# Performance work log

Measured on AMD Instinct MI355X. Metric: run time of the kernel, lower is better.

## Reference

```python
import jax, jax.numpy as jnp
import numpy as np

# (C,H,W) of x0..x11; flattened size +1 homogeneous coordinate per key
SHAPES = [(3,32,32),(96,32,32),(96,32,32),(96,16,16),(192,16,16),(192,16,16),(192,8,8),(192,8,8),(192,8,8),(640,1,1),(100,1,1),(10,1,1)]
# (Cin,Cout,k,stride,pad) for conv1..conv9
CONV = [(3,96,3,1,1),(96,96,3,1,1),(96,96,3,2,1),(96,192,3,1,1),(192,192,3,1,1),(192,192,3,2,1),(192,192,3,1,1),(192,192,1,1,0),(192,10,1,1,0)]
B = 128


def setup_inputs():
    key = jax.random.key(0)
    inp = {}
    k, key = jax.random.split(key)
    inp['x0'] = jax.random.normal(k, (int(np.prod(SHAPES[0])) + 1, B), jnp.float32)
    for i, s in enumerate(SHAPES):
        n = int(np.prod(s)) + 1
        k1, k2, key = jax.random.split(key, 3)
        inp['perm%d' % i] = jax.random.permutation(k1, n)
        inp['diag%d' % i] = jax.random.uniform(k2, (n,), jnp.float32, 0.5, 1.5)
    for j, (ci, co, ks, st, pd) in enumerate(CONV):
        k1, k2, key = jax.random.split(key, 3)
        inp['w%d' % (j + 1)] = jax.random.normal(k1, (co, ci, ks, ks), jnp.float32) / np.float32(np.sqrt(ci * ks * ks))
        inp['b%d' % (j + 1)] = jax.random.normal(k2, (co,), jnp.float32) * 0.01
    k1, k2, k3, k4 = jax.random.split(key, 4)
    inp['fw1'] = jax.random.normal(k1, (100, 640), jnp.float32) / np.float32(np.sqrt(640))
    inp['fb1'] = jax.random.normal(k2, (100,), jnp.float32) * 0.01
    inp['fw2'] = jax.random.normal(k3, (10, 100), jnp.float32) / np.float32(np.sqrt(100))
    inp['fb2'] = jax.random.normal(k4, (10,), jnp.float32) * 0.01
    return inp


def _decode(x, perm, diag):
    # A_inv @ x with A_inv = P^T D^{-1}; P^T gather index is argsort(perm)
    return (x / diag[:, None])[jnp.argsort(perm)]


def _encode(y, perm, diag):
    # A @ y with A = D P; (P y)[i] = y[perm[i]]
    return diag[:, None] * y[perm]


def _conv_aug(v, w, b, shape_in, stride, pad):
    # affine-augmented conv: [W b; 0 1] applied to [feat; t]
    C, H, Wd = shape_in
    feat, t = v[:-1], v[-1]                      # (C*H*W, B), (B,)
    x = feat.T.reshape(-1, C, H, Wd)
    y = jax.lax.conv_general_dilated(x, w, (stride, stride), [(pad, pad), (pad, pad)],
                                     dimension_numbers=('NCHW', 'OIHW', 'NCHW'))
    y = y + b[None, :, None, None] * t[:, None, None, None]
    yf = y.reshape(y.shape[0], -1).T             # (N_out, B)
    return jnp.concatenate([yf, t[None, :]], axis=0)


def _fc_aug(v, w, b):
    feat, t = v[:-1], v[-1]
    return jnp.concatenate([w @ feat + b[:, None] * t[None, :], t[None, :]], axis=0)


def _forward(x0, perms, diags, ws, bs, fw1, fb1, fw2, fb2):
    x = x0
    for i in range(9):
        v = _decode(x, perms[i], diags[i])
        y = _conv_aug(v, ws[i], bs[i], SHAPES[i], CONV[i][3], CONV[i][4])
        x = jax.nn.relu(_encode(y, perms[i + 1], diags[i + 1]))
    v = _decode(x, perms[9], diags[9])
    x = jax.nn.relu(_encode(_fc_aug(v, fw1, fb1), perms[10], diags[10]))
    v = _decode(x, perms[10], diags[10])
    return _encode(_fc_aug(v, fw2, fb2), perms[11], diags[11])


def reference(x0, perm0, perm1, perm2, perm3, perm4, perm5, perm6, perm7, perm8, perm9, perm10, perm11,
              diag0, diag1, diag2, diag3, diag4, diag5, diag6, diag7, diag8, diag9, diag10, diag11,
              w1, b1, w2, b2, w3, b3, w4, b4, w5, b5, w6, b6, w7, b7, w8, b8, w9, b9,
              fw1, fb1, fw2, fb2):
    perms = [perm0, perm1, perm2, perm3, perm4, perm5, perm6, perm7, perm8, perm9, perm10, perm11]
    diags = [diag0, diag1, diag2, diag3, diag4, diag5, diag6, diag7, diag8, diag9, diag10, diag11]
    ws = [w1, w2, w3, w4, w5, w6, w7, w8, w9]
    bs = [b1, b2, b3, b4, b5, b6, b7, b8, b9]
    return _forward(x0, perms, diags, ws, bs, fw1, fb1, fw2, fb2)
```

## Files before the change

### kernel.cpp

```cpp
#include <hip/hip_runtime.h>
#include <stdint.h>


#define B 128
#define ZPAD 2048
#define NBLK 1024
#define NTHR 256
#define JSTRIDE ((NBLK >> 3) * 4)
#define AGT __HIP_MEMORY_SCOPE_AGENT

typedef _Float16 f16_t;
typedef __attribute__((ext_vector_type(8))) _Float16 f16x8;
typedef __attribute__((ext_vector_type(4))) _Float16 f16x4;
typedef __attribute__((ext_vector_type(4))) float f32x4;

struct WArgs {
    const float* w[9]; const float* b[9];
    int Ci[9], Co[9], KS[9], Cp[9], NCG[9];
    int woff[10]; int boff[10];
};

__device__ __forceinline__ int xcc_id() {
    int x;
    asm("s_getreg_b32 %0, hwreg(20, 0, 32)" : "=s"(x));
    return x & 7;
}

__device__ __forceinline__ void gbar(int* bar, int ph) {
    __syncthreads();
    if (threadIdx.x == 0) {
        const int x = xcc_id();
        int* leaf  = bar + x * 32;
        int* ldone = bar + 256 + x * 32;
        int* root  = bar + 512;
        int* cnt   = bar + 544;
        if (ph == 0) {
            for (;;) {
                int s = 0;
#pragma unroll
                for (int k = 0; k < 8; ++k)
                    s += __hip_atomic_load(cnt + k, __ATOMIC_RELAXED, AGT);
                if (s == NBLK) break;
                __builtin_amdgcn_s_sleep(2);
            }
        }
        const int myc = __hip_atomic_load(cnt + x, __ATOMIC_RELAXED, AGT);
        int nact = 0;
#pragma unroll
        for (int k = 0; k < 8; ++k)
            nact += (__hip_atomic_load(cnt + k, __ATOMIC_RELAXED, AGT) != 0) ? 1 : 0;
        int old = __hip_atomic_fetch_add(leaf, 1, __ATOMIC_RELAXED, AGT);
        if (old == (ph + 1) * myc - 1) {
            __builtin_amdgcn_fence(__ATOMIC_RELEASE, "agent");
            __hip_atomic_fetch_add(root, 1, __ATOMIC_RELAXED, AGT);
            while (__hip_atomic_load(root, __ATOMIC_RELAXED, AGT) < (ph + 1) * nact)
                __builtin_amdgcn_s_sleep(8);
            __builtin_amdgcn_fence(__ATOMIC_ACQUIRE, "agent");
            __hip_atomic_store(ldone, ph + 1, __ATOMIC_RELAXED, AGT);
        } else {
            while (__hip_atomic_load(ldone, __ATOMIC_RELAXED, AGT) < ph + 1)
                __builtin_amdgcn_s_sleep(8);
            asm volatile("buffer_inv sc0\n\ts_waitcnt vmcnt(0)" ::: "memory");
        }
    }
    __syncthreads();
}

__device__ void prep_phase(const WArgs& A,
                           const float* __restrict__ x0, const int* __restrict__ perm0,
                           const float* __restrict__ diag0,
                           f16_t* __restrict__ wp, float* __restrict__ bp,
                           f16_t* __restrict__ x8a, f16_t* __restrict__ x8b,
                           float* __restrict__ t0) {
    const int NT = NBLK * NTHR;
    const int gtid = blockIdx.x * NTHR + threadIdx.x;
    for (int idx = gtid; idx < ZPAD; idx += NT) {
        x8a[idx] = (f16_t)0.f; x8b[idx] = (f16_t)0.f;
    }
    for (int idx = gtid; idx < 1024 * 128; idx += NT) {
        int p = idx >> 7, n = idx & 127;
        f16_t* base = x8a + ZPAD + p * 1024 + n * 8;
        base[3] = (f16_t)0.f;
        *(uint64_t*)(base + 4) = 0ull;
    }
    for (int idx = gtid; idx < A.boff[9]; idx += NT) {
        int l = 0;
        while (idx >= A.boff[l + 1]) ++l;
        int co = idx - A.boff[l];
        bp[idx] = (co < A.Co[l]) ? A.b[l][co] : 0.f;
    }
    for (int idx = gtid; idx < A.woff[9]; idx += NT) {
        int l = 0;
        while (idx >= A.woff[l + 1]) ++l;
        int e = idx - A.woff[l];
        int j = e & 7;
        int t1_ = e >> 3;
        int Cp = A.Cp[l];
        int co = t1_ % Cp;
        int gg = t1_ / Cp;
        int ncg = A.NCG[l];
        int tap = gg / ncg, cg = gg - tap * ncg;
        int ks = A.KS[l];
        int kh = tap / ks, kw = tap - kh * ks;
        int ci = cg * 8 + j;
        float val = 0.f;
        if (co < A.Co[l] && tap < ks * ks && ci < A.Ci[l])
            val = A.w[l][(((size_t)co * A.Ci[l] + ci) * ks + kh) * ks + kw];
        wp[idx] = (f16_t)val;
    }
    for (int idx = gtid; idx < 3073 * B; idx += NT) {
        int row = idx >> 7, n = idx & 127;
        int i = perm0[row];
        float val = x0[(size_t)row * B + n] / diag0[row];
        if (i < 3072) {
            int c = i >> 10, pp = i & 1023;
            x8a[ZPAD + pp * 1024 + n * 8 + c] = (f16_t)val;
        } else {
            t0[n] = val;
        }
    }
}

template <int KS, int NS, int NSPLIT, int CB, bool F32OUT,
          int Hi, int Wo_log2, int HWo, int STRD, int PAD,
          int NCG, int NCHUNK, int KGR, int Co, int Cp>
__device__ __forceinline__ void conv_layer(
    const f16_t* __restrict__ xin, const float* __restrict__ t_in,
    const f16_t* __restrict__ wp, const float* __restrict__ bp,
    f16_t* __restrict__ xout, float* __restrict__ t_out, float* __restrict__ f32out)
{
    constexpr int PF = 2;
    constexpr int MS = 4;
    constexpr int Wi = Hi;
    constexpr int PB8 = HWo / 8;
    constexpr int UJ = NSPLIT * CB * PB8;
    constexpr int HiWi = Hi * Wi;
    constexpr int HiWi4 = 4 * HiWi;
    constexpr int NCGHW = NCG * HiWi;
    const int wv = threadIdx.x >> 6;
    const int lane = threadIdx.x & 63;
    const int q = lane >> 4;
    const int r = lane & 15;
    const int X = blockIdx.x & 7;

    if (blockIdx.x == 0 && threadIdx.x < B) {
        float tvv = fmaxf(t_in[threadIdx.x], 0.f);
        if (F32OUT) f32out[(size_t)Co * HWo * B + threadIdx.x] = tvv;
        else        t_out[threadIdx.x] = tvv;
    }

    for (int j = (blockIdx.x >> 3) * 4 + wv; j < UJ; j += JSTRIDE) {
        int nh = 0, j2 = j;
        if (NSPLIT > 1) { nh = j % NSPLIT; j2 = j / NSPLIT; }
        const int cog = (CB > 1) ? (j2 % CB) : 0;
        const int jp  = (CB > 1) ? (j2 / CB) : j2;
        const int p = X * PB8 + jp;
        const int co0 = cog * 64;
        const int ncol0 = nh * (NS * 16);
        const int ncol8 = ncol0 * 8;
        const int ho = p >> Wo_log2;
        const int wo = p & ((1 << Wo_log2) - 1);
        const f16_t* xdata = xin + ZPAD;

        float tv[NS];
#pragma unroll
        for (int ns = 0; ns < NS; ++ns) tv[ns] = t_in[ncol0 + ns * 16 + r];

        f32x4 acc[MS][NS];
#pragma unroll
        for (int ms = 0; ms < MS; ++ms) {
            float4 b4 = *(const float4*)(bp + co0 + ms * 16 + q * 4);
#pragma unroll
            for (int ns = 0; ns < NS; ++ns) {
                acc[ms][ns][0] = b4.x * tv[ns];
                acc[ms][ns][1] = b4.y * tv[ns];
                acc[ms][ns][2] = b4.z * tv[ns];
                acc[ms][ns][3] = b4.w * tv[ns];
            }
        }

        const int hb = ho * STRD - PAD, wb = wo * STRD - PAD;
        const int wend = wb + KS;

        int g = q, cg = q, hi = hb, wi = wb, cgHW;
        {
            while (cg >= NCG) { cg -= NCG; ++wi; if (wi == wend) { wi = wb; ++hi; } }
            cgHW = cg * HiWi;
        }

        f16x8 bf[PF][NS], af[PF][MS];

        auto advance = [&]() {
            g += 4; cg += 4; cgHW += HiWi4;
            if constexpr (NCG >= 4) {
                int c2 = cg - NCG;
                bool wrap = c2 >= 0;
                int wn = wi + 1;
                bool ww = wrap & (wn == wend);
                cg   = wrap ? c2 : cg;
                cgHW = wrap ? cgHW - NCGHW : cgHW;
                wi   = wrap ? (ww ? wb : wn) : wi;
                hi   = ww ? hi + 1 : hi;
            } else {
                while (cg >= NCG) { cg -= NCG; cgHW -= NCGHW; ++wi; if (wi == wend) { wi = wb; ++hi; } }
            }
        };
        auto loadB = [&](f16x8* bb8) {
            bool v = (g < KGR) & ((unsigned)hi < (unsigned)Hi) & ((unsigned)wi < (unsigned)Wi);
            int boff = (cgHW + hi * Wi + wi) << 10;
            const f16_t* bb = xdata + (v ? boff : -ZPAD) + ncol8 + r * 8;
#pragma unroll
            for (int ns = 0; ns < NS; ++ns) bb8[ns] = *(const f16x8*)(bb + ns * 128);
        };
        auto loadA = [&](f16x8* a, int c) {
            int ac = c < NCHUNK ? c : NCHUNK - 1;
            const f16_t* ap = wp + (((ac * 4 + q) * Cp) + co0 + r) * 8;
#pragma unroll
            for (int ms = 0; ms < MS; ++ms) a[ms] = *(const f16x8*)(ap + ms * 128);
        };
        auto domfma = [&](f16x8* a, f16x8* bb8) {
#pragma unroll
            for (int ms = 0; ms < MS; ++ms)
#pragma unroll
                for (int ns = 0; ns < NS; ++ns)
                    acc[ms][ns] = __builtin_amdgcn_mfma_f32_16x16x32_f16(a[ms], bb8[ns], acc[ms][ns], 0, 0, 0);
        };

#pragma unroll
        for (int pf = 0; pf < PF; ++pf) { loadB(bf[pf]); loadA(af[pf], pf); advance(); }
        constexpr int nck = ((NCHUNK + PF - 1) / PF) * PF;
        for (int c = 0; c < nck; c += PF) {
#pragma unroll
            for (int pf = 0; pf < PF; ++pf) {
                domfma(af[pf], bf[pf]);
                loadB(bf[pf]); loadA(af[pf], c + PF + pf); advance();
            }
        }

        if constexpr (!F32OUT) {
#pragma unroll
            for (int ms = 0; ms < MS; ++ms) {
                int cob = co0 + ms * 16 + q * 4;
                if (cob < Co) {
                    int off0 = ((cob >> 3) * HWo + p) * 1024 + (cob & 7) + ncol8 + r * 8;
#pragma unroll
                    for (int ns = 0; ns < NS; ++ns) {
                        f16x4 h;
                        h[0] = (f16_t)fmaxf(acc[ms][ns][0], 0.f);
                        h[1] = (f16_t)fmaxf(acc[ms][ns][1], 0.f);
                        h[2] = (f16_t)fmaxf(acc[ms][ns][2], 0.f);
                        h[3] = (f16_t)fmaxf(acc[ms][ns][3], 0.f);
                        *(f16x4*)(xout + ZPAD + off0 + ns * 128) = h;
                    }
                }
            }
        } else {
#pragma unroll
            for (int ms = 0; ms < MS; ++ms)
#pragma unroll
                for (int ns = 0; ns < NS; ++ns)
#pragma unroll
                    for (int e = 0; e < 4; ++e) {
                        int co = co0 + ms * 16 + q * 4 + e;
                        if (co < Co)
                            f32out[((size_t)co * HWo + p) * B + ncol0 + ns * 16 + r] =
                                fmaxf(acc[ms][ns][e], 0.f);
                    }
        }
    }
}

__device__ __forceinline__ void fc_phase(const float* __restrict__ v, const float* __restrict__ w,
                                         const float* __restrict__ b, float* __restrict__ y,
                                         int K, int R, bool do_relu) {
    if (threadIdx.x >= B) return;
    int r = blockIdx.x;
    int n = threadIdx.x;
    float t = v[(size_t)K * B + n];
    float val;
    if (r == R) {
        val = t;
    } else {
        float a0 = 0.f, a1 = 0.f, a2 = 0.f, a3 = 0.f;
        float a4 = 0.f, a5 = 0.f, a6 = 0.f, a7 = 0.f;
        const float* wr = w + (size_t)r * K;
        int k = 0;
        for (; k + 8 <= K; k += 8) {
            float4 w0 = *(const float4*)(wr + k);
            float4 w1 = *(const float4*)(wr + k + 4);
            float x0 = v[(size_t)(k + 0) * B + n];
            float x1 = v[(size_t)(k + 1) * B + n];
            float x2 = v[(size_t)(k + 2) * B + n];
            float x3 = v[(size_t)(k + 3) * B + n];
            float x4 = v[(size_t)(k + 4) * B + n];
            float x5 = v[(size_t)(k + 5) * B + n];
            float x6 = v[(size_t)(k + 6) * B + n];
            float x7 = v[(size_t)(k + 7) * B + n];
            a0 = fmaf(w0.x, x0, a0);
            a1 = fmaf(w0.y, x1, a1);
            a2 = fmaf(w0.z, x2, a2);
            a3 = fmaf(w0.w, x3, a3);
            a4 = fmaf(w1.x, x4, a4);
            a5 = fmaf(w1.y, x5, a5);
            a6 = fmaf(w1.z, x6, a6);
            a7 = fmaf(w1.w, x7, a7);
        }
        for (; k < K; ++k)
            a0 = fmaf(wr[k], v[(size_t)k * B + n], a0);
        val = b[r] * t + ((a0 + a1) + (a2 + a3)) + ((a4 + a5) + (a6 + a7));
    }
    if (do_relu) val = fmaxf(val, 0.f);
    y[(size_t)r * B + n] = val;
}

__device__ __forceinline__ void fc2_phase(const float* __restrict__ v, const float* __restrict__ w,
                                          const float* __restrict__ b, const int* __restrict__ perm,
                                          const float* __restrict__ diag, float* __restrict__ out) {
    if (threadIdx.x >= B) return;
    int jrow = blockIdx.x;
    int n = threadIdx.x;
    int r = perm[jrow];
    float d = diag[jrow];
    float t = v[100 * B + n];
    float val;
    if (r == 10) {
        val = t;
    } else {
        float a0 = 0.f, a1 = 0.f, a2 = 0.f, a3 = 0.f;
        const float* wr = w + (size_t)r * 100;
        for (int k = 0; k < 100; k += 4) {
            float4 w4 = *(const float4*)(wr + k);
            a0 = fmaf(w4.x, v[(size_t)(k + 0) * B + n], a0);
            a1 = fmaf(w4.y, v[(size_t)(k + 1) * B + n], a1);
            a2 = fmaf(w4.z, v[(size_t)(k + 2) * B + n], a2);
            a3 = fmaf(w4.w, v[(size_t)(k + 3) * B + n], a3);
        }
        val = b[r] * t + (a0 + a1) + (a2 + a3);
    }
    out[(size_t)jrow * B + n] = d * val;
}

__global__ __launch_bounds__(NTHR, 4) void meganet_kernel(
    WArgs A,
    const float* __restrict__ x0, const int* __restrict__ perm0, const float* __restrict__ diag0,
    const int* __restrict__ perm11, const float* __restrict__ diag11,
    const float* __restrict__ fw1, const float* __restrict__ fb1,
    const float* __restrict__ fw2, const float* __restrict__ fb2,
    f16_t* wp, float* bp, f16_t* x8a, f16_t* x8b,
    float* t0, float* t1, float* bufA, float* bufB, float* out, int* bar)
{
    if (threadIdx.x == 0)
        __hip_atomic_fetch_add(bar + 544 + xcc_id(), 1, __ATOMIC_RELAXED, AGT);

    prep_phase(A, x0, perm0, diag0, wp, bp, x8a, x8b, t0);
    gbar(bar, 0);
    conv_layer<3, 2, 4, 2, false, 32, 5, 1024, 1, 1,  1,  3,   9,  96, 128>(
        x8a, t0, wp + A.woff[0], bp + A.boff[0], x8b, t1, nullptr);
    gbar(bar, 1);
    conv_layer<3, 2, 4, 2, false, 32, 5, 1024, 1, 1, 12, 27, 108,  96, 128>(
        x8b, t1, wp + A.woff[1], bp + A.boff[1], x8a, t0, nullptr);
    gbar(bar, 2);
    conv_layer<3, 1, 8, 2, false, 32, 4,  256, 2, 1, 12, 27, 108,  96, 128>(
        x8a, t0, wp + A.woff[2], bp + A.boff[2], x8b, t1, nullptr);
    gbar(bar, 3);
    conv_layer<3, 2, 4, 3, false, 16, 4,  256, 1, 1, 12, 27, 108, 192, 192>(
        x8b, t1, wp + A.woff[3], bp + A.boff[3], x8a, t0, nullptr);
    gbar(bar, 4);
    conv_layer<3, 2, 4, 3, false, 16, 4,  256, 1, 1, 24, 54, 216, 192, 192>(
        x8a, t0, wp + A.woff[4], bp + A.boff[4], x8b, t1, nullptr);
    gbar(bar, 5);
    conv_layer<3, 1, 8, 3, false, 16, 3,   64, 2, 1, 24, 54, 216, 192, 192>(
        x8b, t1, wp + A.woff[5], bp + A.boff[5], x8a, t0, nullptr);
    gbar(bar, 6);
    conv_layer<3, 1, 8, 3, false,  8, 3,   64, 1, 1, 24, 54, 216, 192, 192>(
        x8a, t0, wp + A.woff[6], bp + A.boff[6], x8b, t1, nullptr);
    gbar(bar, 7);
    conv_layer<1, 1, 8, 3, false,  8, 3,   64, 1, 0, 24,  6,  24, 192, 192>(
        x8b, t1, wp + A.woff[7], bp + A.boff[7], x8a, t0, nullptr);
    gbar(bar, 8);
    conv_layer<1, 1, 8, 1, true,   8, 3,   64, 1, 0, 24,  6,  24,  10,  64>(
        x8a, t0, wp + A.woff[8], bp + A.boff[8], nullptr, nullptr, bufA);
    gbar(bar, 9);
    if (blockIdx.x <= 100) fc_phase(bufA, fw1, fb1, bufB, 640, 100, true);
    gbar(bar, 10);
    if (blockIdx.x < 11) fc2_phase(bufB, fw2, fb2, perm11, diag11, out);
}


extern "C" void kernel_launch(void* const* d_in, const int* in_sizes, int n_in,
                              void* d_out, int out_size, void* d_ws, size_t ws_size,
                              hipStream_t stream) {
    const float* x0 = (const float*)d_in[0];
    const int*   perm[12];
    const float* diag[12];
    for (int i = 0; i < 12; ++i) {
        perm[i] = (const int*)d_in[1 + 2 * i];
        diag[i] = (const float*)d_in[2 + 2 * i];
    }
    const float* wts[9];
    const float* bia[9];
    for (int j = 0; j < 9; ++j) {
        wts[j] = (const float*)d_in[25 + 2 * j];
        bia[j] = (const float*)d_in[26 + 2 * j];
    }
    const float* fw1 = (const float*)d_in[43];
    const float* fb1 = (const float*)d_in[44];
    const float* fw2 = (const float*)d_in[45];
    const float* fb2 = (const float*)d_in[46];
    float* out = (float*)d_out;

    static const int CiA[9]  = {3, 96, 96, 96, 192, 192, 192, 192, 192};
    static const int CoA[9]  = {96, 96, 96, 192, 192, 192, 192, 192, 10};
    static const int KSA[9]  = {3, 3, 3, 3, 3, 3, 3, 1, 1};
    static const int CpA[9]  = {128, 128, 128, 192, 192, 192, 192, 192, 64};
    static const int NCGA[9] = {1, 12, 12, 12, 24, 24, 24, 24, 24};
    static const int NCHK[9] = {3, 27, 27, 27, 54, 54, 54, 6, 6};

    char* wsb = (char*)d_ws;
    const size_t BUF_F32  = 1574912;
    const size_t X8_BYTES = (size_t)(ZPAD + 12 * 1024 * 1024) * 2;
    float* bufA = (float*)wsb;
    float* bufB = (float*)(wsb + BUF_F32);
    f16_t* x8a  = (f16_t*)(wsb + 2 * BUF_F32);
    f16_t* x8b  = (f16_t*)(wsb + 2 * BUF_F32 + X8_BYTES);
    f16_t* wpb  = (f16_t*)(wsb + 2 * BUF_F32 + 2 * X8_BYTES);
    const size_t WP_BYTES = 2888704;
    float* bpb  = (float*)(wsb + 2 * BUF_F32 + 2 * X8_BYTES + WP_BYTES);
    float* t0   = (float*)((char*)bpb + 8192);
    float* t1   = t0 + 256;
    int*   bar  = (int*)((char*)bpb + 12288);

    WArgs WA;
    int wo = 0, bo = 0;
    for (int l = 0; l < 9; ++l) {
        WA.w[l] = wts[l]; WA.b[l] = bia[l];
        WA.Ci[l] = CiA[l]; WA.Co[l] = CoA[l]; WA.KS[l] = KSA[l];
        WA.Cp[l] = CpA[l]; WA.NCG[l] = NCGA[l];
        WA.woff[l] = wo; wo += NCHK[l] * 4 * CpA[l] * 8;
        WA.boff[l] = bo; bo += CpA[l];
    }
    WA.woff[9] = wo; WA.boff[9] = bo;

    hipMemsetAsync(bar, 0, 4096, stream);

    meganet_kernel<<<NBLK, NTHR, 0, stream>>>(
        WA, x0, perm[0], diag[0], perm[11], diag[11],
        fw1, fb1, fw2, fb2,
        wpb, bpb, x8a, x8b, t0, t1, bufA, bufB, out, bar);
}
```

Before: 385.4 us.

## Add a mid level to the grid barrier tree and split FC1 reduction across threads

The per-XCC leaf counter of the grid barrier is replaced by a three-level tree. Blocks first atomically increment a mid counter shared by groups of 8 slots. Only the last arriver of each group bumps the XCC leaf counter, and then the root. This is meant to reduce atomic contention on a single counter at each of the eleven barriers, at the cost of an extra atomic hop and workgroup-scope atomics whose cross-CU visibility relies on the shared L2. Separately, the FC1 phase now uses all 256 threads, splitting K in two halves and combining the partial sums through shared memory, so half the threads no longer sit idle.

```diff
diff --git a/kernel.cpp b/kernel.cpp
--- a/kernel.cpp
+++ b/kernel.cpp
@@ -8,6 +8,7 @@
 #define NTHR 256
 #define JSTRIDE ((NBLK >> 3) * 4)
 #define AGT __HIP_MEMORY_SCOPE_AGENT
+#define WGS __HIP_MEMORY_SCOPE_WORKGROUP
 
 typedef _Float16 f16_t;
 typedef __attribute__((ext_vector_type(8))) _Float16 f16x8;
@@ -26,14 +27,12 @@
     return x & 7;
 }
 
-__device__ __forceinline__ void gbar(int* bar, int ph) {
+__device__ __forceinline__ void gbar(int* bar, int ph, int slot) {
     __syncthreads();
     if (threadIdx.x == 0) {
         const int x = xcc_id();
-        int* leaf  = bar + x * 32;
-        int* ldone = bar + 256 + x * 32;
-        int* root  = bar + 512;
-        int* cnt   = bar + 544;
+        int* root = bar + 4608;
+        int* cnt  = bar + 4640;
         if (ph == 0) {
             for (;;) {
                 int s = 0;
@@ -49,8 +48,19 @@
 #pragma unroll
         for (int k = 0; k < 8; ++k)
             nact += (__hip_atomic_load(cnt + k, __ATOMIC_RELAXED, AGT) != 0) ? 1 : 0;
-        int old = __hip_atomic_fetch_add(leaf, 1, __ATOMIC_RELAXED, AGT);
-        if (old == (ph + 1) * myc - 1) {
+        const int m  = slot >> 3;
+        const int mc = min(8, myc - m * 8);
+        const int nm = (myc + 7) >> 3;
+        int* mid   = bar + (x * 16 + m) * 32;
+        int* leaf  = bar + 4096 + x * 32;
+        int* ldone = bar + 4352 + x * 32;
+        bool last = false;
+        int mo = __hip_atomic_fetch_add(mid, 1, __ATOMIC_RELAXED, WGS);
+        if (mo == (ph + 1) * mc - 1) {
+            int lo = __hip_atomic_fetch_add(leaf, 1, __ATOMIC_RELAXED, WGS);
+            last = (lo == (ph + 1) * nm - 1);
+        }
+        if (last) {
             __builtin_amdgcn_fence(__ATOMIC_RELEASE, "agent");
             __hip_atomic_fetch_add(root, 1, __ATOMIC_RELAXED, AGT);
             while (__hip_atomic_load(root, __ATOMIC_RELAXED, AGT) < (ph + 1) * nact)
@@ -270,47 +280,38 @@
     }
 }
 
-__device__ __forceinline__ void fc_phase(const float* __restrict__ v, const float* __restrict__ w,
-                                         const float* __restrict__ b, float* __restrict__ y,
-                                         int K, int R, bool do_relu) {
-    if (threadIdx.x >= B) return;
+__device__ __forceinline__ void fc1_phase(const float* __restrict__ v, const float* __restrict__ w,
+                                          const float* __restrict__ b, float* __restrict__ y,
+                                          float* __restrict__ red) {
     int r = blockIdx.x;
-    int n = threadIdx.x;
-    float t = v[(size_t)K * B + n];
-    float val;
-    if (r == R) {
-        val = t;
-    } else {
-        float a0 = 0.f, a1 = 0.f, a2 = 0.f, a3 = 0.f;
-        float a4 = 0.f, a5 = 0.f, a6 = 0.f, a7 = 0.f;
-        const float* wr = w + (size_t)r * K;
-        int k = 0;
-        for (; k + 8 <= K; k += 8) {
+    int n = threadIdx.x & 127;
+    int kh = threadIdx.x >> 7;
+    float t = v[640 * B + n];
+    float a0 = 0.f, a1 = 0.f, a2 = 0.f, a3 = 0.f;
+    float a4 = 0.f, a5 = 0.f, a6 = 0.f, a7 = 0.f;
+    if (r != 100) {
+        const float* wr = w + (size_t)r * 640 + kh * 320;
+        const float* vr = v + (size_t)kh * 320 * B + n;
+        for (int k = 0; k < 320; k += 8) {
             float4 w0 = *(const float4*)(wr + k);
             float4 w1 = *(const float4*)(wr + k + 4);
-            float x0 = v[(size_t)(k + 0) * B + n];
-            float x1 = v[(size_t)(k + 1) * B + n];
-            float x2 = v[(size_t)(k + 2) * B + n];
-            float x3 = v[(size_t)(k + 3) * B + n];
-            float x4 = v[(size_t)(k + 4) * B + n];
-            float x5 = v[(size_t)(k + 5) * B + n];
-            float x6 = v[(size_t)(k + 6) * B + n];
-            float x7 = v[(size_t)(k + 7) * B + n];
-            a0 = fmaf(w0.x, x0, a0);
-            a1 = fmaf(w0.y, x1, a1);
-            a2 = fmaf(w0.z, x2, a2);
-            a3 = fmaf(w0.w, x3, a3);
-            a4 = fmaf(w1.x, x4, a4);
-            a5 = fmaf(w1.y, x5, a5);
-            a6 = fmaf(w1.z, x6, a6);
-            a7 = fmaf(w1.w, x7, a7);
-        }
-        for (; k < K; ++k)
-            a0 = fmaf(wr[k], v[(size_t)k * B + n], a0);
-        val = b[r] * t + ((a0 + a1) + (a2 + a3)) + ((a4 + a5) + (a6 + a7));
-    }
-    if (do_relu) val = fmaxf(val, 0.f);
-    y[(size_t)r * B + n] = val;
+            a0 = fmaf(w0.x, vr[(k + 0) * B], a0);
+            a1 = fmaf(w0.y, vr[(k + 1) * B], a1);
+            a2 = fmaf(w0.z, vr[(k + 2) * B], a2);
+            a3 = fmaf(w0.w, vr[(k + 3) * B], a3);
+            a4 = fmaf(w1.x, vr[(k + 4) * B], a4);
+            a5 = fmaf(w1.y, vr[(k + 5) * B], a5);
+            a6 = fmaf(w1.z, vr[(k + 6) * B], a6);
+            a7 = fmaf(w1.w, vr[(k + 7) * B], a7);
+        }
+    }
+    float part = ((a0 + a1) + (a2 + a3)) + ((a4 + a5) + (a6 + a7));
+    if (kh) red[n] = part;
+    __syncthreads();
+    if (!kh) {
+        float val = (r == 100) ? t : b[r] * t + part + red[n];
+        y[(size_t)r * B + n] = fmaxf(val, 0.f);
+    }
 }
 
 __device__ __forceinline__ void fc2_phase(const float* __restrict__ v, const float* __restrict__ w,
@@ -349,40 +350,42 @@
     f16_t* wp, float* bp, f16_t* x8a, f16_t* x8b,
     float* t0, float* t1, float* bufA, float* bufB, float* out, int* bar)
 {
+    __shared__ float red[128];
+    int slot = 0;
     if (threadIdx.x == 0)
-        __hip_atomic_fetch_add(bar + 544 + xcc_id(), 1, __ATOMIC_RELAXED, AGT);
+        slot = __hip_atomic_fetch_add(bar + 4640 + xcc_id(), 1, __ATOMIC_RELAXED, AGT);
 
     prep_phase(A, x0, perm0, diag0, wp, bp, x8a, x8b, t0);
-    gbar(bar, 0);
+    gbar(bar, 0, slot);
     conv_layer<3, 2, 4, 2, false, 32, 5, 1024, 1, 1,  1,  3,   9,  96, 128>(
         x8a, t0, wp + A.woff[0], bp + A.boff[0], x8b, t1, nullptr);
-    gbar(bar, 1);
+    gbar(bar, 1, slot);
     conv_layer<3, 2, 4, 2, false, 32, 5, 1024, 1, 1, 12, 27, 108,  96, 128>(
         x8b, t1, wp + A.woff[1], bp + A.boff[1], x8a, t0, nullptr);
-    gbar(bar, 2);
+    gbar(bar, 2, slot);
     conv_layer<3, 1, 8, 2, false, 32, 4,  256, 2, 1, 12, 27, 108,  96, 128>(
         x8a, t0, wp + A.woff[2], bp + A.boff[2], x8b, t1, nullptr);
-    gbar(bar, 3);
+    gbar(bar, 3, slot);
     conv_layer<3, 2, 4, 3, false, 16, 4,  256, 1, 1, 12, 27, 108, 192, 192>(
         x8b, t1, wp + A.woff[3], bp + A.boff[3], x8a, t0, nullptr);
-    gbar(bar, 4);
+    gbar(bar, 4, slot);
     conv_layer<3, 2, 4, 3, false, 16, 4,  256, 1, 1, 24, 54, 216, 192, 192>(
         x8a, t0, wp + A.woff[4], bp + A.boff[4], x8b, t1, nullptr);
-    gbar(bar, 5);
+    gbar(bar, 5, slot);
     conv_layer<3, 1, 8, 3, false, 16, 3,   64, 2, 1, 24, 54, 216, 192, 192>(
         x8b, t1, wp + A.woff[5], bp + A.boff[5], x8a, t0, nullptr);
-    gbar(bar, 6);
+    gbar(bar, 6, slot);
     conv_layer<3, 1, 8, 3, false,  8, 3,   64, 1, 1, 24, 54, 216, 192, 192>(
         x8a, t0, wp + A.woff[6], bp + A.boff[6], x8b, t1, nullptr);
-    gbar(bar, 7);
+    gbar(bar, 7, slot);
     conv_layer<1, 1, 8, 3, false,  8, 3,   64, 1, 0, 24,  6,  24, 192, 192>(
         x8b, t1, wp + A.woff[7], bp + A.boff[7], x8a, t0, nullptr);
-    gbar(bar, 8);
+    gbar(bar, 8, slot);
     conv_layer<1, 1, 8, 1, true,   8, 3,   64, 1, 0, 24,  6,  24,  10,  64>(
         x8a, t0, wp + A.woff[8], bp + A.boff[8], nullptr, nullptr, bufA);
-    gbar(bar, 9);
-    if (blockIdx.x <= 100) fc_phase(bufA, fw1, fb1, bufB, 640, 100, true);
-    gbar(bar, 10);
+    gbar(bar, 9, slot);
+    if (blockIdx.x <= 100) fc1_phase(bufA, fw1, fb1, bufB, red);
+    gbar(bar, 10, slot);
     if (blockIdx.x < 11) fc2_phase(bufB, fw2, fb2, perm11, diag11, out);
 }
 
@@ -441,7 +444,7 @@
     }
     WA.woff[9] = wo; WA.boff[9] = bo;
 
-    hipMemsetAsync(bar, 0, 4096, stream);
+    hipMemsetAsync(bar, 0, 20480, stream);
 
     meganet_kernel<<<NBLK, NTHR, 0, stream>>>(
         WA, x0, perm[0], diag[0], perm[11], diag[11],
```

Result: no change. 389.7 us (+1.1%).
